# Kernel optimization log

Measured on AMD Instinct MI355X. Metric: run time of the kernel, lower is better.

## Reference

```python
import jax, jax.numpy as jnp
import numpy as np
from jax import lax

K = 3
EPS = 1e-5


def get_graph_feature(x, k):
    # Faithful to the torch code, including flat .view() reshapes (no transpose)
    B, N = x.shape[0], x.shape[1]          # num_points = x.size(1)
    x = x.reshape(B, -1, N)                # (B, C, N) flat reshape
    C = x.shape[1]
    inner = -2.0 * jnp.einsum('bcn,bcm->bnm', x, x)           # (B, N, N)
    xx = jnp.sum(x * x, axis=1, keepdims=True)                # (B, 1, N)
    dist = -xx - inner - jnp.swapaxes(xx, 1, 2)               # neg sq distances
    idx = lax.top_k(dist, k)[1]                               # (B, N, k) nearest
    flat = x.reshape(B * N, C)                                # flat reshape (as torch .view)
    idx_full = (idx + (jnp.arange(B) * N)[:, None, None]).reshape(-1)
    feature = flat[idx_full].reshape(B, N, k, C)
    xc = x.reshape(B, N, 1, C)                                # flat reshape (as torch .view)
    feature = jnp.concatenate([feature - xc, jnp.broadcast_to(xc, (B, N, k, C))], axis=3)
    return feature.reshape(B, 2 * C, k, N)                    # flat reshape (as torch .view)


def bn(h, g, b, m, v, axis):
    shape = [1] * h.ndim
    shape[axis] = -1
    inv = g.reshape(shape) / jnp.sqrt(v.reshape(shape) + EPS)
    return (h - m.reshape(shape)) * inv + b.reshape(shape)


def setup_inputs() -> dict:
    key = jax.random.key(0)
    ks = jax.random.split(key, 24)
    B, N = 8, 4096

    def bn_params(i, c):
        return {
            f'bn{i}_g': jax.random.uniform(ks[4 * (ord(i) % 4)], (c,), jnp.float32) + 0.5,
            f'bn{i}_b': jax.random.normal(jax.random.fold_in(key, 10 + ord(i)), (c,), jnp.float32) * 0.1,
            f'bn{i}_m': jax.random.normal(jax.random.fold_in(key, 20 + ord(i)), (c,), jnp.float32) * 0.1,
            f'bn{i}_v': jax.random.uniform(jax.random.fold_in(key, 30 + ord(i)), (c,), jnp.float32) + 0.5,
        }

    inp = {
        'x': jax.random.normal(ks[0], (B, N, 3), jnp.float32),
        'w1': jax.random.normal(ks[1], (64, 6), jnp.float32) * (1.0 / np.sqrt(6.0)),
        'wA': jax.random.normal(ks[2], (256, 82), jnp.float32) * (1.0 / np.sqrt(82.0)),
        'bA': jax.random.normal(ks[3], (256,), jnp.float32) * 0.01,
        'wB': jax.random.normal(ks[4], (128, 256), jnp.float32) * (1.0 / np.sqrt(256.0)),
        'bB': jax.random.normal(ks[5], (128,), jnp.float32) * 0.01,
        'wC': jax.random.normal(ks[6], (3, 128), jnp.float32) * (1.0 / np.sqrt(128.0)),
        'bC': jax.random.normal(ks[7], (3,), jnp.float32) * 0.01,
    }
    inp.update(bn_params('1', 64))
    inp.update(bn_params('A', 256))
    inp.update(bn_params('B', 128))
    return inp


def reference(x, w1, wA, bA, wB, bB, wC, bC,
              bn1_g, bn1_b, bn1_m, bn1_v,
              bnA_g, bnA_b, bnA_m, bnA_v,
              bnB_g, bnB_b, bnB_m, bnB_v):
    f = get_graph_feature(x, K)                         # (B, 6, K, N)
    h = jnp.einsum('oc,bckn->bokn', w1, f)              # 1x1 conv, no bias
    h = jax.nn.leaky_relu(bn(h, bn1_g, bn1_b, bn1_m, bn1_v, 1), 0.2)
    x1 = jnp.max(h, axis=-1)                            # (B, 64, K)  (max over N!)
    x2 = jnp.max(get_graph_feature(x1, K), axis=-1)     # (B, 6, K)   (conv2 unused in source)
    x3 = jnp.max(get_graph_feature(x2, K), axis=-1)     # (B, 6, K)
    x4 = jnp.max(get_graph_feature(x3, K), axis=-1)     # (B, 6, K)
    xc = jnp.concatenate([x1, x2, x3, x4], axis=1)      # (B, 82, K)
    p = jnp.max(xc, axis=-1)                            # adaptive_max_pool1d -> (B, 82)
    h = jax.nn.leaky_relu(bn(p @ wA.T + bA, bnA_g, bnA_b, bnA_m, bnA_v, 1), 0.2)
    h = jax.nn.leaky_relu(bn(h @ wB.T + bB, bnB_g, bnB_b, bnB_m, bnB_v, 1), 0.2)
    return jax.nn.softmax(h @ wC.T + bC, axis=1)        # (B, 3)
```

## Files before the change

### kernel.cpp

```cpp
#include <hip/hip_runtime.h>
#include <math.h>

#define NPTS 4096
#define EPSV 1e-5f

__global__ __launch_bounds__(512, 4) void k_knn1(const float* __restrict__ x,
                                                 int* __restrict__ idx1) {
  __shared__ float4 pts[NPTS];
  __shared__ float cd[64][8][3];
  __shared__ int   ci[64][8][3];
  const int b   = blockIdx.x >> 6;
  const int blk = blockIdx.x & 63;
  const float* xb = x + b * (NPTS * 3);
  const int t = threadIdx.x;

  for (int m = t; m < NPTS; m += 512) {
    float a0 = xb[m], a1 = xb[NPTS + m], a2 = xb[2 * NPTS + m];
    float xx = a0 * a0; xx = fmaf(a1, a1, xx); xx = fmaf(a2, a2, xx);
    pts[m] = make_float4(a0, a1, a2, xx);
  }
  __syncthreads();

  const int p = t & 63;
  const int s = t >> 6;
  const int n = blk * 64 + p;
  const float4 pn = pts[n];
  const float p2x = 2.0f * pn.x, p2y = 2.0f * pn.y, p2z = 2.0f * pn.z;
  const float c0 = -pn.w;
  float d0 = -INFINITY, d1 = -INFINITY, d2 = -INFINITY;
  int   i0 = 0x7fffffff, i1 = 0x7fffffff, i2 = 0x7fffffff;
  const int mstart = s * 512;

  float4 qa[8];
#pragma unroll
  for (int j = 0; j < 8; ++j) qa[j] = pts[mstart + j];

  for (int mb = 0; mb < 512; mb += 16) {
    float4 qb[8];
#pragma unroll
    for (int j = 0; j < 8; ++j) qb[j] = pts[mstart + mb + 8 + j];
#pragma unroll
    for (int j = 0; j < 8; ++j) {
      float4 q = qa[j];
      float d = fmaf(p2x, q.x, fmaf(p2y, q.y, fmaf(p2z, q.z, c0))) - q.w;
      if (d > d2) {
        int m = mstart + mb + j;
        bool g1 = d > d1, g0 = d > d0;
        d2 = g1 ? d1 : d;               i2 = g1 ? i1 : m;
        d1 = g0 ? d0 : (g1 ? d : d1);   i1 = g0 ? i0 : (g1 ? m : i1);
        d0 = g0 ? d : d0;               i0 = g0 ? m : i0;
      }
    }
#pragma unroll
    for (int j = 0; j < 8; ++j) qa[j] = pts[mstart + ((mb + 16 + j) & 511)];
#pragma unroll
    for (int j = 0; j < 8; ++j) {
      float4 q = qb[j];
      float d = fmaf(p2x, q.x, fmaf(p2y, q.y, fmaf(p2z, q.z, c0))) - q.w;
      if (d > d2) {
        int m = mstart + mb + 8 + j;
        bool g1 = d > d1, g0 = d > d0;
        d2 = g1 ? d1 : d;               i2 = g1 ? i1 : m;
        d1 = g0 ? d0 : (g1 ? d : d1);   i1 = g0 ? i0 : (g1 ? m : i1);
        d0 = g0 ? d : d0;               i0 = g0 ? m : i0;
      }
    }
  }

  cd[p][s][0] = d0; cd[p][s][1] = d1; cd[p][s][2] = d2;
  ci[p][s][0] = i0; ci[p][s][1] = i1; ci[p][s][2] = i2;
  __syncthreads();

  if (t < 64) {
    int* op = idx1 + (b * NPTS + blk * 64 + t) * 3;
    float pd = INFINITY; int pi = -1;
    for (int r = 0; r < 3; ++r) {
      float bd = -INFINITY; int bi = 0x7fffffff;
      for (int sc = 0; sc < 8; ++sc) {
        for (int kk = 0; kk < 3; ++kk) {
          float dv = cd[t][sc][kk]; int iv = ci[t][sc][kk];
          bool allowed = (dv < pd) || (dv == pd && iv > pi);
          bool better  = (dv > bd) || (dv == bd && iv < bi);
          if (allowed && better) { bd = dv; bi = iv; }
        }
      }
      op[r] = bi;
      pd = bd; pi = bi;
    }
  }
}

__global__ __launch_bounds__(256, 2) void k_convmax(const float* __restrict__ x,
                                                    const int* __restrict__ idx1,
                                                    const float* __restrict__ w1,
                                                    float* __restrict__ pmax) {
  __shared__ float  xs[12288];
  __shared__ float4 Ft4[128][2];
  __shared__ float  w1s[384];
  __shared__ float  smax[4][64];
  const int b    = blockIdx.x / 96;
  const int rr   = blockIdx.x - b * 96;
  const int kk   = rr >> 5;
  const int tile = rr & 31;
  const int t = threadIdx.x;
  for (int i = t; i < 384; i += 256) w1s[i] = w1[i];
  {
    const float4* xb4 = (const float4*)(x + b * 12288);
    float4* xs4 = (float4*)xs;
#pragma unroll
    for (int i = 0; i < 12; ++i) xs4[t + 256 * i] = xb4[t + 256 * i];
  }
  const int* ib = idx1 + b * 12288;
  __syncthreads();

  const int tn = t & 127, ch = t >> 7;
  const int n = tile * 128 + tn;
  float* ftrow = (float*)&Ft4[tn][0];
#pragma unroll
  for (int j = 0; j < 3; ++j) {
    int c = ch * 3 + j;
    int ofs = c * 12288 + kk * 4096 + n;
    int np  = ofs / 18;
    int rem = ofs - np * 18;
    int kp  = rem / 6;
    int cp  = rem - kp * 6;
    float val;
    if (cp < 3) {
      int jj = ib[np * 3 + kp];
      val = xs[jj * 3 + cp] - xs[np * 3 + cp];
    } else {
      val = xs[np * 3 + cp - 3];
    }
    ftrow[c] = val;
  }
  __syncthreads();

  const int o = t & 63, sub = t >> 6;
  float w[6];
#pragma unroll
  for (int c = 0; c < 6; ++c) w[c] = w1s[o * 6 + c];
  const int base = sub * 32;
  float mx = -INFINITY;

  float4 ra[4][2];
#pragma unroll
  for (int r = 0; r < 4; ++r) { ra[r][0] = Ft4[base + r][0]; ra[r][1] = Ft4[base + r][1]; }

  for (int i = 0; i < 32; i += 8) {
    float4 rb[4][2];
#pragma unroll
    for (int r = 0; r < 4; ++r) {
      rb[r][0] = Ft4[base + i + 4 + r][0];
      rb[r][1] = Ft4[base + i + 4 + r][1];
    }
#pragma unroll
    for (int r = 0; r < 4; ++r) {
      float h = w[0] * ra[r][0].x;
      h = fmaf(w[1], ra[r][0].y, h);
      h = fmaf(w[2], ra[r][0].z, h);
      h = fmaf(w[3], ra[r][0].w, h);
      h = fmaf(w[4], ra[r][1].x, h);
      h = fmaf(w[5], ra[r][1].y, h);
      mx = fmaxf(mx, h);
    }
#pragma unroll
    for (int r = 0; r < 4; ++r) {
      int nr = base + ((i + 8 + r) & 31);
      ra[r][0] = Ft4[nr][0]; ra[r][1] = Ft4[nr][1];
    }
#pragma unroll
    for (int r = 0; r < 4; ++r) {
      float h = w[0] * rb[r][0].x;
      h = fmaf(w[1], rb[r][0].y, h);
      h = fmaf(w[2], rb[r][0].z, h);
      h = fmaf(w[3], rb[r][0].w, h);
      h = fmaf(w[4], rb[r][1].x, h);
      h = fmaf(w[5], rb[r][1].y, h);
      mx = fmaxf(mx, h);
    }
  }
  smax[sub][o] = mx;
  __syncthreads();
  if (t < 64) {
    float m01 = fmaxf(smax[0][t], smax[1][t]);
    float m23 = fmaxf(smax[2][t], smax[3][t]);
    pmax[((b * 3 + kk) * 64 + t) * 32 + tile] = fmaxf(m01, m23);
  }
}

__device__ __forceinline__ void top3_insert(float d, int m,
                                            float& d0, float& d1, float& d2,
                                            int& i0, int& i1, int& i2) {
  if (d > d2) {
    bool g1 = d > d1;
    bool g0 = d > d0;
    d2 = g1 ? d1 : d;                 i2 = g1 ? i1 : m;
    d1 = g0 ? d0 : (g1 ? d : d1);     i1 = g0 ? i0 : (g1 ? m : i1);
    d0 = g0 ? d : d0;                 i0 = g0 ? m : i0;
  }
}

__global__ __launch_bounds__(256) void k_tail(
    const float* __restrict__ pmax,
    const float* __restrict__ bn1g, const float* __restrict__ bn1b,
    const float* __restrict__ bn1m, const float* __restrict__ bn1v,
    const float* __restrict__ wA, const float* __restrict__ bA,
    const float* __restrict__ bnAg, const float* __restrict__ bnAb,
    const float* __restrict__ bnAm, const float* __restrict__ bnAv,
    const float* __restrict__ wB, const float* __restrict__ bB,
    const float* __restrict__ bnBg, const float* __restrict__ bnBb,
    const float* __restrict__ bnBm, const float* __restrict__ bnBv,
    const float* __restrict__ wC, const float* __restrict__ bC,
    float* __restrict__ out) {
  __shared__ float a1[192];
  __shared__ int   idx2[192];
  __shared__ float a2[18], a3[18], a4[18];
  __shared__ int   idxs[18];
  __shared__ float pv[82];
  __shared__ float hA[256];
  __shared__ float hB[128];
  __shared__ float lg[3];
  const int b = blockIdx.x;
  const int t = threadIdx.x;

  if (t < 192) {
    int o = t / 3, k = t - o * 3;
    const float4* p4 = (const float4*)(pmax + ((b * 3 + k) * 64 + o) * 32);
    float4 v[8];
#pragma unroll
    for (int j = 0; j < 8; ++j) v[j] = p4[j];
    float mx = -INFINITY;
#pragma unroll
    for (int j = 0; j < 8; ++j) {
      mx = fmaxf(mx, fmaxf(fmaxf(v[j].x, v[j].y), fmaxf(v[j].z, v[j].w)));
    }
    float inv = bn1g[o] / sqrtf(bn1v[o] + EPSV);
    float val = (mx - bn1m[o]) * inv + bn1b[o];
    a1[o * 3 + k] = val >= 0.f ? val : 0.2f * val;
  }
  __syncthreads();

  if (t < 64) {
    float px = a1[t], py = a1[64 + t], pz = a1[128 + t];
    float pp = px * px; pp = fmaf(py, py, pp); pp = fmaf(pz, pz, pp);
    float d0 = -INFINITY, d1 = -INFINITY, d2 = -INFINITY;
    int i0 = 0, i1 = 0, i2 = 0;
#pragma unroll 8
    for (int m = 0; m < 64; ++m) {
      float qx = a1[m], qy = a1[64 + m], qz = a1[128 + m];
      float qq = qx * qx; qq = fmaf(qy, qy, qq); qq = fmaf(qz, qz, qq);
      float dot = px * qx; dot = fmaf(py, qy, dot); dot = fmaf(pz, qz, dot);
      float d = 2.f * dot - pp - qq;
      top3_insert(d, m, d0, d1, d2, i0, i1, i2);
    }
    idx2[t * 3 + 0] = i0; idx2[t * 3 + 1] = i1; idx2[t * 3 + 2] = i2;
  }
  __syncthreads();

  if (t < 18) {
    int o = t / 3, kk = t - o * 3;
    float mx = -INFINITY;
#pragma unroll 8
    for (int nn = 0; nn < 64; ++nn) {
      int ofs = o * 192 + kk * 64 + nn;
      int np = ofs / 18; int rem = ofs - np * 18;
      int kp = rem / 6;  int cp  = rem - kp * 6;
      float val = (cp < 3) ? (a1[idx2[np * 3 + kp] * 3 + cp] - a1[np * 3 + cp])
                           : a1[np * 3 + cp - 3];
      mx = fmaxf(mx, val);
    }
    a2[t] = mx;
  }
  __syncthreads();

  for (int stage = 0; stage < 2; ++stage) {
    const float* src = (stage == 0) ? a2 : a3;
    float*       dst = (stage == 0) ? a3 : a4;
    if (t < 6) {
      float px = src[t], py = src[6 + t], pz = src[12 + t];
      float pp = px * px; pp = fmaf(py, py, pp); pp = fmaf(pz, pz, pp);
      float d0 = -INFINITY, d1 = -INFINITY, d2 = -INFINITY;
      int i0 = 0, i1 = 0, i2 = 0;
#pragma unroll
      for (int m = 0; m < 6; ++m) {
        float qx = src[m], qy = src[6 + m], qz = src[12 + m];
        float qq = qx * qx; qq = fmaf(qy, qy, qq); qq = fmaf(qz, qz, qq);
        float dot = px * qx; dot = fmaf(py, qy, dot); dot = fmaf(pz, qz, dot);
        float d = 2.f * dot - pp - qq;
        top3_insert(d, m, d0, d1, d2, i0, i1, i2);
      }
      idxs[t * 3 + 0] = i0; idxs[t * 3 + 1] = i1; idxs[t * 3 + 2] = i2;
    }
    __syncthreads();
    if (t < 18) {
      int o = t / 3, kk = t - o * 3;
      float mx = -INFINITY;
#pragma unroll
      for (int nn = 0; nn < 6; ++nn) {
        int ofs = o * 18 + kk * 6 + nn;
        int np = ofs / 18; int rem = ofs - np * 18;
        int kp = rem / 6;  int cp  = rem - kp * 6;
        float val = (cp < 3) ? (src[idxs[np * 3 + kp] * 3 + cp] - src[np * 3 + cp])
                             : src[np * 3 + cp - 3];
        mx = fmaxf(mx, val);
      }
      dst[t] = mx;
    }
    __syncthreads();
  }

  if (t < 82) {
    float mx;
    if (t < 64)      { int o = t;      mx = fmaxf(fmaxf(a1[o*3], a1[o*3+1]), a1[o*3+2]); }
    else if (t < 70) { int o = t - 64; mx = fmaxf(fmaxf(a2[o*3], a2[o*3+1]), a2[o*3+2]); }
    else if (t < 76) { int o = t - 70; mx = fmaxf(fmaxf(a3[o*3], a3[o*3+1]), a3[o*3+2]); }
    else             { int o = t - 76; mx = fmaxf(fmaxf(a4[o*3], a4[o*3+1]), a4[o*3+2]); }
    pv[t] = mx;
  }
  __syncthreads();

  {
    float acc = bA[t];
    const float* wr = wA + t * 82;
#pragma unroll 8
    for (int i = 0; i < 82; ++i) acc = fmaf(wr[i], pv[i], acc);
    float inv = bnAg[t] / sqrtf(bnAv[t] + EPSV);
    float v = (acc - bnAm[t]) * inv + bnAb[t];
    hA[t] = v >= 0.f ? v : 0.2f * v;
  }
  __syncthreads();

  if (t < 128) {
    float acc = bB[t];
    const float4* wr4 = (const float4*)(wB + t * 256);
#pragma unroll 8
    for (int i = 0; i < 64; ++i) {
      float4 wv = wr4[i];
      acc = fmaf(wv.x, hA[4 * i + 0], acc);
      acc = fmaf(wv.y, hA[4 * i + 1], acc);
      acc = fmaf(wv.z, hA[4 * i + 2], acc);
      acc = fmaf(wv.w, hA[4 * i + 3], acc);
    }
    float inv = bnBg[t] / sqrtf(bnBv[t] + EPSV);
    float v = (acc - bnBm[t]) * inv + bnBb[t];
    hB[t] = v >= 0.f ? v : 0.2f * v;
  }
  __syncthreads();

  if (t < 3) {
    float acc = bC[t];
    const float* wr = wC + t * 128;
#pragma unroll 8
    for (int i = 0; i < 128; ++i) acc = fmaf(wr[i], hB[i], acc);
    lg[t] = acc;
  }
  __syncthreads();
  if (t == 0) {
    float m = fmaxf(fmaxf(lg[0], lg[1]), lg[2]);
    float e0 = expf(lg[0] - m), e1 = expf(lg[1] - m), e2 = expf(lg[2] - m);
    float s = e0 + e1 + e2;
    out[b * 3 + 0] = e0 / s;
    out[b * 3 + 1] = e1 / s;
    out[b * 3 + 2] = e2 / s;
  }
}

extern "C" void kernel_launch(void* const* d_in, const int* in_sizes, int n_in,
                              void* d_out, int out_size, void* d_ws, size_t ws_size,
                              hipStream_t stream) {
  (void)in_sizes; (void)n_in; (void)out_size; (void)ws_size;
  const float* x    = (const float*)d_in[0];
  const float* w1   = (const float*)d_in[1];
  const float* wA   = (const float*)d_in[2];
  const float* bA   = (const float*)d_in[3];
  const float* wB   = (const float*)d_in[4];
  const float* bB   = (const float*)d_in[5];
  const float* wC   = (const float*)d_in[6];
  const float* bC   = (const float*)d_in[7];
  const float* bn1g = (const float*)d_in[8];
  const float* bn1b = (const float*)d_in[9];
  const float* bn1m = (const float*)d_in[10];
  const float* bn1v = (const float*)d_in[11];
  const float* bnAg = (const float*)d_in[12];
  const float* bnAb = (const float*)d_in[13];
  const float* bnAm = (const float*)d_in[14];
  const float* bnAv = (const float*)d_in[15];
  const float* bnBg = (const float*)d_in[16];
  const float* bnBb = (const float*)d_in[17];
  const float* bnBm = (const float*)d_in[18];
  const float* bnBv = (const float*)d_in[19];
  float* out = (float*)d_out;

  int*   idx1 = (int*)d_ws;
  float* pmax = (float*)((char*)d_ws + 8 * 4096 * 3 * 4);

  k_knn1<<<512, 512, 0, stream>>>(x, idx1);
  k_convmax<<<768, 256, 0, stream>>>(x, idx1, w1, pmax);
  k_tail<<<8, 256, 0, stream>>>(pmax,
                                bn1g, bn1b, bn1m, bn1v,
                                wA, bA, bnAg, bnAb, bnAm, bnAv,
                                wB, bB, bnBg, bnBb, bnBm, bnBv,
                                wC, bC, out);
}
```

Baseline: 181.6 us.

## Halve kNN block size, branch top-3 insert, and gather conv inputs from global

The kNN kernel now runs 256 threads per block, with each of four sub-threads per point scanning 1024 candidates instead of eight scanning 512. The top-3 insert becomes a nested branch that skips extra work when the new distance only beats the third slot. The point buffer is padded so the prefetch can read past the chunk end without a wraparound mask. The conv/max kernel drops its 48KB shared-memory staging of the whole batch and gathers its few needed values straight from global/L2, which should cut shared-memory use and the barrier, at the cost of uncoalesced gathers.

```diff
diff --git a/kernel.cpp b/kernel.cpp
--- a/kernel.cpp
+++ b/kernel.cpp
@@ -4,17 +4,17 @@
 #define NPTS 4096
 #define EPSV 1e-5f
 
-__global__ __launch_bounds__(512, 4) void k_knn1(const float* __restrict__ x,
+__global__ __launch_bounds__(256, 2) void k_knn1(const float* __restrict__ x,
                                                  int* __restrict__ idx1) {
-  __shared__ float4 pts[NPTS];
-  __shared__ float cd[64][8][3];
-  __shared__ int   ci[64][8][3];
+  __shared__ float4 pts[NPTS + 8];
+  __shared__ float cd[64][4][3];
+  __shared__ int   ci[64][4][3];
   const int b   = blockIdx.x >> 6;
   const int blk = blockIdx.x & 63;
   const float* xb = x + b * (NPTS * 3);
   const int t = threadIdx.x;
 
-  for (int m = t; m < NPTS; m += 512) {
+  for (int m = t; m < NPTS; m += 256) {
     float a0 = xb[m], a1 = xb[NPTS + m], a2 = xb[2 * NPTS + m];
     float xx = a0 * a0; xx = fmaf(a1, a1, xx); xx = fmaf(a2, a2, xx);
     pts[m] = make_float4(a0, a1, a2, xx);
@@ -29,40 +29,49 @@
   const float c0 = -pn.w;
   float d0 = -INFINITY, d1 = -INFINITY, d2 = -INFINITY;
   int   i0 = 0x7fffffff, i1 = 0x7fffffff, i2 = 0x7fffffff;
-  const int mstart = s * 512;
+  const int mstart = s * 1024;
+  const float4* __restrict__ pchunk = &pts[mstart];
 
   float4 qa[8];
 #pragma unroll
-  for (int j = 0; j < 8; ++j) qa[j] = pts[mstart + j];
-
-  for (int mb = 0; mb < 512; mb += 16) {
+  for (int j = 0; j < 8; ++j) qa[j] = pchunk[j];
+
+  for (int mb = 0; mb < 1024; mb += 16) {
     float4 qb[8];
 #pragma unroll
-    for (int j = 0; j < 8; ++j) qb[j] = pts[mstart + mb + 8 + j];
+    for (int j = 0; j < 8; ++j) qb[j] = pchunk[mb + 8 + j];
 #pragma unroll
     for (int j = 0; j < 8; ++j) {
       float4 q = qa[j];
       float d = fmaf(p2x, q.x, fmaf(p2y, q.y, fmaf(p2z, q.z, c0))) - q.w;
       if (d > d2) {
         int m = mstart + mb + j;
-        bool g1 = d > d1, g0 = d > d0;
-        d2 = g1 ? d1 : d;               i2 = g1 ? i1 : m;
-        d1 = g0 ? d0 : (g1 ? d : d1);   i1 = g0 ? i0 : (g1 ? m : i1);
-        d0 = g0 ? d : d0;               i0 = g0 ? m : i0;
+        if (d > d1) {
+          bool g0 = d > d0;
+          d2 = d1;            i2 = i1;
+          d1 = g0 ? d0 : d;   i1 = g0 ? i0 : m;
+          d0 = g0 ? d : d0;   i0 = g0 ? m : i0;
+        } else {
+          d2 = d; i2 = m;
+        }
       }
     }
 #pragma unroll
-    for (int j = 0; j < 8; ++j) qa[j] = pts[mstart + ((mb + 16 + j) & 511)];
+    for (int j = 0; j < 8; ++j) qa[j] = pchunk[mb + 16 + j];
 #pragma unroll
     for (int j = 0; j < 8; ++j) {
       float4 q = qb[j];
       float d = fmaf(p2x, q.x, fmaf(p2y, q.y, fmaf(p2z, q.z, c0))) - q.w;
       if (d > d2) {
         int m = mstart + mb + 8 + j;
-        bool g1 = d > d1, g0 = d > d0;
-        d2 = g1 ? d1 : d;               i2 = g1 ? i1 : m;
-        d1 = g0 ? d0 : (g1 ? d : d1);   i1 = g0 ? i0 : (g1 ? m : i1);
-        d0 = g0 ? d : d0;               i0 = g0 ? m : i0;
+        if (d > d1) {
+          bool g0 = d > d0;
+          d2 = d1;            i2 = i1;
+          d1 = g0 ? d0 : d;   i1 = g0 ? i0 : m;
+          d0 = g0 ? d : d0;   i0 = g0 ? m : i0;
+        } else {
+          d2 = d; i2 = m;
+        }
       }
     }
   }
@@ -76,7 +85,7 @@
     float pd = INFINITY; int pi = -1;
     for (int r = 0; r < 3; ++r) {
       float bd = -INFINITY; int bi = 0x7fffffff;
-      for (int sc = 0; sc < 8; ++sc) {
+      for (int sc = 0; sc < 4; ++sc) {
         for (int kk = 0; kk < 3; ++kk) {
           float dv = cd[t][sc][kk]; int iv = ci[t][sc][kk];
           bool allowed = (dv < pd) || (dv == pd && iv > pi);
@@ -90,11 +99,10 @@
   }
 }
 
-__global__ __launch_bounds__(256, 2) void k_convmax(const float* __restrict__ x,
-                                                    const int* __restrict__ idx1,
-                                                    const float* __restrict__ w1,
-                                                    float* __restrict__ pmax) {
-  __shared__ float  xs[12288];
+__global__ __launch_bounds__(256) void k_convmax(const float* __restrict__ x,
+                                                 const int* __restrict__ idx1,
+                                                 const float* __restrict__ w1,
+                                                 float* __restrict__ pmax) {
   __shared__ float4 Ft4[128][2];
   __shared__ float  w1s[384];
   __shared__ float  smax[4][64];
@@ -104,14 +112,8 @@
   const int tile = rr & 31;
   const int t = threadIdx.x;
   for (int i = t; i < 384; i += 256) w1s[i] = w1[i];
-  {
-    const float4* xb4 = (const float4*)(x + b * 12288);
-    float4* xs4 = (float4*)xs;
-#pragma unroll
-    for (int i = 0; i < 12; ++i) xs4[t + 256 * i] = xb4[t + 256 * i];
-  }
-  const int* ib = idx1 + b * 12288;
-  __syncthreads();
+  const float* xb = x + b * 12288;
+  const int*   ib = idx1 + b * 12288;
 
   const int tn = t & 127, ch = t >> 7;
   const int n = tile * 128 + tn;
@@ -127,9 +129,9 @@
     float val;
     if (cp < 3) {
       int jj = ib[np * 3 + kp];
-      val = xs[jj * 3 + cp] - xs[np * 3 + cp];
+      val = xb[jj * 3 + cp] - xb[np * 3 + cp];
     } else {
-      val = xs[np * 3 + cp - 3];
+      val = xb[np * 3 + cp - 3];
     }
     ftrow[c] = val;
   }
@@ -394,7 +396,7 @@
   int*   idx1 = (int*)d_ws;
   float* pmax = (float*)((char*)d_ws + 8 * 4096 * 3 * 4);
 
-  k_knn1<<<512, 512, 0, stream>>>(x, idx1);
+  k_knn1<<<512, 256, 0, stream>>>(x, idx1);
   k_convmax<<<768, 256, 0, stream>>>(x, idx1, w1, pmax);
   k_tail<<<8, 256, 0, stream>>>(pmax,
                                 bn1g, bn1b, bn1m, bn1v,
```

After: 192.1 us. 5.8% more time.
